# Kernel tuning notes

Measured on AMD Instinct MI355X. Metric: run time of the kernel, lower is better.

## Reference

```python
import jax, jax.numpy as jnp
import numpy as np


def setup_inputs() -> dict:
    key = jax.random.key(0)
    kq, kk, kv = jax.random.split(key, 3)
    B, H, S, D = 4, 16, 2048, 64
    q = jax.random.normal(kq, (B, H, S, D), dtype=jnp.float32)
    k = jax.random.normal(kk, (B, H, S, D), dtype=jnp.float32)
    v = jax.random.normal(kv, (B, H, S, D), dtype=jnp.float32)
    return {"q": q, "k": k, "v": v}


def reference(q, k, v):
    # SplitScaleAttend (inference, no mask, no dropout):
    # softmax(q k^T / sqrt(d)) v — the chunked loop in the original is a
    # memory-saving schedule of the same math, so one fused expression here.
    scale = q.shape[-1] ** (-0.5)
    # (b h i d),(b h j d) -> (b h i j)
    sim = jnp.einsum("bhid,bhjd->bhij", q, k * scale)
    attn = jax.nn.softmax(sim, axis=-1)
    # (b h i j),(b h j d) -> (b h i d)
    return jnp.einsum("bhij,bhjd->bhid", attn, v)
```

## Files before the change

### kernel.cpp

```cpp
#include <hip/hip_runtime.h>
#include <hip/hip_bf16.h>

typedef __attribute__((ext_vector_type(8))) short short8_t;
typedef __attribute__((ext_vector_type(4))) float f32x4;
typedef __attribute__((ext_vector_type(16))) float f32x16;
typedef __attribute__((ext_vector_type(4))) unsigned u32x4;

static constexpr int B = 4, H = 16, S = 2048, D = 64;
static constexpr int WAVES = 8, QW = 64, QBLK = WAVES * QW;
static constexpr int KVBLK = 64, NT = S / KVBLK;
static constexpr int LDK = 72;

#define QSCALE 0.18033688011112042f

__device__ __forceinline__ unsigned pk2(float a, float b) {
    __hip_bfloat162 h = __float22bfloat162_rn(float2{a, b});
    unsigned u;
    __builtin_memcpy(&u, &h, 4);
    return u;
}

__device__ __forceinline__ float fexp2(float x) {
#if __has_builtin(__builtin_amdgcn_exp2f)
    return __builtin_amdgcn_exp2f(x);
#else
    return exp2f(x);
#endif
}

__device__ __forceinline__ float frcp(float x) {
#if __has_builtin(__builtin_amdgcn_rcpf)
    return __builtin_amdgcn_rcpf(x);
#else
    return 1.f / x;
#endif
}

#define QK_MFMA(KH, S0, S1)                                                              \
    do {                                                                                 \
        _Pragma("unroll")                                                                \
        for (int kc = 0; kc < 4; ++kc) {                                                 \
            const short8_t ka = *reinterpret_cast<const short8_t*>(                      \
                &Ks[cb][(KH) * 32 + ql][kc * 16 + hi * 8]);                              \
            S0 = __builtin_amdgcn_mfma_f32_32x32x16_bf16(ka, qf0[kc], S0, 0, 0, 0);      \
            S1 = __builtin_amdgcn_mfma_f32_32x32x16_bf16(ka, qf1[kc], S1, 0, 0, 0);      \
        }                                                                                \
    } while (0)

#define EXP_SUM_PACK(S0, S1, CD0, CD1)                                                   \
    do {                                                                                 \
        float a0 = 0.f, a1 = 0.f, b0 = 0.f, b1 = 0.f;                                    \
        _Pragma("unroll")                                                                \
        for (int r = 0; r < 16; ++r) {                                                   \
            const float e = fexp2(S0[r]);                                                \
            S0[r] = e;                                                                   \
            if (r & 1) a1 += e; else a0 += e;                                            \
        }                                                                                \
        _Pragma("unroll")                                                                \
        for (int r = 0; r < 16; ++r) {                                                   \
            const float e = fexp2(S1[r]);                                                \
            S1[r] = e;                                                                   \
            if (r & 1) b1 += e; else b0 += e;                                            \
        }                                                                                \
        l0_r += a0 + a1;                                                                 \
        l1_r += b0 + b1;                                                                 \
        _Pragma("unroll")                                                                \
        for (int jj = 0; jj < 8; ++jj) {                                                 \
            CD0[jj] = pk2(S0[jj * 2], S0[jj * 2 + 1]);                                   \
            CD1[jj] = pk2(S1[jj * 2], S1[jj * 2 + 1]);                                   \
        }                                                                                \
    } while (0)

#define PV2(CD0, CD1, KS)                                                                \
    do {                                                                                 \
        const int h_ = (KS) & 1;                                                         \
        const short8_t vfa =                                                             \
            *reinterpret_cast<const short8_t*>(&Vt[cb][ql][(KS) * 16 + hi * 8]);         \
        const short8_t vfb =                                                             \
            *reinterpret_cast<const short8_t*>(&Vt[cb][32 + ql][(KS) * 16 + hi * 8]);    \
        {                                                                                \
            unsigned x0 = CD0[4 * h_ + 0], y0 = CD0[4 * h_ + 2];                         \
            unsigned x1 = CD0[4 * h_ + 1], y1 = CD0[4 * h_ + 3];                         \
            asm volatile("v_permlane32_swap_b32 %0, %1" : "+v"(x0), "+v"(y0));           \
            asm volatile("v_permlane32_swap_b32 %0, %1" : "+v"(x1), "+v"(y1));           \
            const u32x4 pu = {x0, x1, y0, y1};                                           \
            const short8_t pa = __builtin_bit_cast(short8_t, pu);                        \
            Od00 = __builtin_amdgcn_mfma_f32_32x32x16_bf16(pa, vfa, Od00, 0, 0, 0);      \
            Od01 = __builtin_amdgcn_mfma_f32_32x32x16_bf16(pa, vfb, Od01, 0, 0, 0);      \
        }                                                                                \
        {                                                                                \
            unsigned x0 = CD1[4 * h_ + 0], y0 = CD1[4 * h_ + 2];                         \
            unsigned x1 = CD1[4 * h_ + 1], y1 = CD1[4 * h_ + 3];                         \
            asm volatile("v_permlane32_swap_b32 %0, %1" : "+v"(x0), "+v"(y0));           \
            asm volatile("v_permlane32_swap_b32 %0, %1" : "+v"(x1), "+v"(y1));           \
            const u32x4 pu = {x0, x1, y0, y1};                                           \
            const short8_t pa = __builtin_bit_cast(short8_t, pu);                        \
            Od10 = __builtin_amdgcn_mfma_f32_32x32x16_bf16(pa, vfa, Od10, 0, 0, 0);      \
            Od11 = __builtin_amdgcn_mfma_f32_32x32x16_bf16(pa, vfb, Od11, 0, 0, 0);      \
        }                                                                                \
    } while (0)

__global__ void __launch_bounds__(512, 2)
attn_fwd(const float* __restrict__ q, const float* __restrict__ k,
         const float* __restrict__ v, float* __restrict__ out) {
    __shared__ short Ks[2][KVBLK][LDK];
    __shared__ short Vt[2][D][LDK];
    __shared__ float Xl[WAVES][2][32];

    const int tid  = threadIdx.x;
    const int lane = tid & 63;
    const int ql   = lane & 31;
    const int hi   = lane >> 5;
    const int wave = tid >> 6;

    const int lid = blockIdx.x;
    const int bh  = (lid & 7) | ((lid >> 5) << 3);
    const int qx  = (lid >> 3) & 3;

    const long base = (long)bh * S * D;
    const int  q0w  = qx * QBLK + wave * QW;

    short8_t qf0[4], qf1[4];
    #pragma unroll
    for (int qb = 0; qb < 2; ++qb) {
        const float* qp = q + base + (long)(q0w + qb * 32 + ql) * D;
        #pragma unroll
        for (int kc = 0; kc < 4; ++kc) {
            const f32x4 a = *reinterpret_cast<const f32x4*>(qp + kc * 16 + hi * 8);
            const f32x4 b = *reinterpret_cast<const f32x4*>(qp + kc * 16 + hi * 8 + 4);
            const u32x4 u = {pk2(a[0] * QSCALE, a[1] * QSCALE),
                             pk2(a[2] * QSCALE, a[3] * QSCALE),
                             pk2(b[0] * QSCALE, b[1] * QSCALE),
                             pk2(b[2] * QSCALE, b[3] * QSCALE)};
            if (qb == 0) qf0[kc] = __builtin_bit_cast(short8_t, u);
            else         qf1[kc] = __builtin_bit_cast(short8_t, u);
        }
    }

    f32x16 Od00, Od01, Od10, Od11;
    #pragma unroll
    for (int r = 0; r < 16; ++r) {
        Od00[r] = 0.f; Od01[r] = 0.f;
        Od10[r] = 0.f; Od11[r] = 0.f;
    }
    float l0_r = 0.f, l1_r = 0.f;

    const int kr  = tid >> 3,       kc0 = (tid & 7) * 8;
    const int vk2 = (tid & 31) * 2, vd0 = (tid >> 5) * 4;
    const float* kptr  = k + base + (long)kr * D + kc0;
    const float* vptrA = v + base + (long)vk2 * D + vd0;

    f32x4 kfa = *reinterpret_cast<const f32x4*>(kptr);
    f32x4 kfb = *reinterpret_cast<const f32x4*>(kptr + 4);
    f32x4 vfa0 = *reinterpret_cast<const f32x4*>(vptrA);
    f32x4 vfb0 = *reinterpret_cast<const f32x4*>(vptrA + D);

    for (int t = 0; t < NT; ++t) {
        const int cb = t & 1;
        {
            const u32x4 ku = {pk2(kfa[0], kfa[1]), pk2(kfa[2], kfa[3]),
                              pk2(kfb[0], kfb[1]), pk2(kfb[2], kfb[3])};
            *reinterpret_cast<u32x4*>(&Ks[cb][kr][kc0]) = ku;
            #pragma unroll
            for (int j = 0; j < 4; ++j) {
                *reinterpret_cast<unsigned*>(&Vt[cb][vd0 + j][vk2]) = pk2(vfa0[j], vfb0[j]);
            }
        }
        __syncthreads();

        if (t + 1 < NT) {
            kptr  += KVBLK * D;
            vptrA += KVBLK * D;
            kfa = *reinterpret_cast<const f32x4*>(kptr);
            kfb = *reinterpret_cast<const f32x4*>(kptr + 4);
            vfa0 = *reinterpret_cast<const f32x4*>(vptrA);
            vfb0 = *reinterpret_cast<const f32x4*>(vptrA + D);
        }

        f32x16 sA0, sA1, sB0, sB1;
        #pragma unroll
        for (int r = 0; r < 16; ++r) { sA0[r] = 0.f; sA1[r] = 0.f; sB0[r] = 0.f; sB1[r] = 0.f; }
        QK_MFMA(0, sA0, sA1);
        QK_MFMA(1, sB0, sB1);

        unsigned cdA0[8], cdA1[8];
        EXP_SUM_PACK(sA0, sA1, cdA0, cdA1);
        PV2(cdA0, cdA1, 0);
        PV2(cdA0, cdA1, 1);

        unsigned cdB0[8], cdB1[8];
        EXP_SUM_PACK(sB0, sB1, cdB0, cdB1);
        PV2(cdB0, cdB1, 2);
        PV2(cdB0, cdB1, 3);
    }

    {
        const float l0m = l0_r + __shfl_xor(l0_r, 32, 64);
        const float l1m = l1_r + __shfl_xor(l1_r, 32, 64);
        if (hi == 0) {
            Xl[wave][0][ql] = frcp(l0m);
            Xl[wave][1][ql] = frcp(l1m);
        }
        float* op = out + base + (long)q0w * D + ql;
        #pragma unroll
        for (int r = 0; r < 16; ++r) {
            const int   row = (r & 3) + 8 * (r >> 2) + 4 * hi;
            const float s   = Xl[wave][0][row];
            op[(long)row * D]      = Od00[r] * s;
            op[(long)row * D + 32] = Od01[r] * s;
        }
        float* op1 = op + 32 * D;
        #pragma unroll
        for (int r = 0; r < 16; ++r) {
            const int   row = (r & 3) + 8 * (r >> 2) + 4 * hi;
            const float s   = Xl[wave][1][row];
            op1[(long)row * D]      = Od10[r] * s;
            op1[(long)row * D + 32] = Od11[r] * s;
        }
    }
}

extern "C" void kernel_launch(void* const* d_in, const int* in_sizes, int n_in,
                              void* d_out, int out_size, void* d_ws, size_t ws_size,
                              hipStream_t stream) {
    const float* q = (const float*)d_in[0];
    const float* k = (const float*)d_in[1];
    const float* v = (const float*)d_in[2];
    float* out = (float*)d_out;
    attn_fwd<<<dim3((S / QBLK) * B * H), 512, 0, stream>>>(q, k, v, out);
}
```

Baseline: 86.24 us.

## Split KV range across two blocks and combine partial outputs in a second kernel

Splits each query block's key/value sequence into two halves processed by separate blocks, doubling the grid to fill more CU slots. Each half writes unnormalized partial outputs in bf16 and row sums to a workspace, and a combine kernel adds them and normalizes. The aim is to lift occupancy and utilization on the large GPU. The cost is extra workspace traffic, an extra launch and bf16 rounding of the partials. The new path is used only when a large enough workspace is provided.

Measured after the change: 100.4 us. 1.16x slower.

```diff
diff --git a/kernel.cpp b/kernel.cpp
--- a/kernel.cpp
+++ b/kernel.cpp
@@ -2,6 +2,7 @@
 #include <hip/hip_bf16.h>
 
 typedef __attribute__((ext_vector_type(8))) short short8_t;
+typedef __attribute__((ext_vector_type(4))) short short4_t;
 typedef __attribute__((ext_vector_type(4))) float f32x4;
 typedef __attribute__((ext_vector_type(16))) float f32x16;
 typedef __attribute__((ext_vector_type(4))) unsigned u32x4;
@@ -9,7 +10,13 @@
 static constexpr int B = 4, H = 16, S = 2048, D = 64;
 static constexpr int WAVES = 8, QW = 64, QBLK = WAVES * QW;
 static constexpr int KVBLK = 64, NT = S / KVBLK;
+static constexpr int NTH = NT / 2;
 static constexpr int LDK = 72;
+
+static constexpr long   ROWS        = (long)B * H * S;
+static constexpr size_t OPART_BYTES = 2ul * ROWS * 64 * 2;
+static constexpr size_t L_OFF       = OPART_BYTES;
+static constexpr size_t WS_NEED     = L_OFF + 2ul * ROWS * 4;
 
 #define QSCALE 0.18033688011112042f
 
@@ -18,6 +25,18 @@
     unsigned u;
     __builtin_memcpy(&u, &h, 4);
     return u;
+}
+__device__ __forceinline__ short bf1(float a) {
+    __hip_bfloat16 h = __float2bfloat16(a);
+    short s;
+    __builtin_memcpy(&s, &h, 2);
+    return s;
+}
+__device__ __forceinline__ float bf2f(short s) {
+    const unsigned u = ((unsigned)(unsigned short)s) << 16;
+    float f;
+    __builtin_memcpy(&f, &u, 4);
+    return f;
 }
 
 __device__ __forceinline__ float fexp2(float x) {
@@ -100,6 +119,139 @@
         }                                                                                \
     } while (0)
 
+#define ATTN_BODY(NTILES, KVOFF)                                                         \
+    short8_t qf0[4], qf1[4];                                                             \
+    _Pragma("unroll")                                                                    \
+    for (int qb = 0; qb < 2; ++qb) {                                                     \
+        const float* qp = q + base + (long)(q0w + qb * 32 + ql) * D;                     \
+        _Pragma("unroll")                                                                \
+        for (int kc = 0; kc < 4; ++kc) {                                                 \
+            const f32x4 a = *reinterpret_cast<const f32x4*>(qp + kc * 16 + hi * 8);      \
+            const f32x4 b = *reinterpret_cast<const f32x4*>(qp + kc * 16 + hi * 8 + 4);  \
+            const u32x4 u = {pk2(a[0] * QSCALE, a[1] * QSCALE),                          \
+                             pk2(a[2] * QSCALE, a[3] * QSCALE),                          \
+                             pk2(b[0] * QSCALE, b[1] * QSCALE),                          \
+                             pk2(b[2] * QSCALE, b[3] * QSCALE)};                         \
+            if (qb == 0) qf0[kc] = __builtin_bit_cast(short8_t, u);                      \
+            else         qf1[kc] = __builtin_bit_cast(short8_t, u);                      \
+        }                                                                                \
+    }                                                                                    \
+    _Pragma("unroll")                                                                    \
+    for (int r = 0; r < 16; ++r) {                                                       \
+        Od00[r] = 0.f; Od01[r] = 0.f;                                                    \
+        Od10[r] = 0.f; Od11[r] = 0.f;                                                    \
+    }                                                                                    \
+    const int kr  = tid >> 3,       kc0 = (tid & 7) * 8;                                 \
+    const int vk2 = (tid & 31) * 2, vd0 = (tid >> 5) * 4;                                \
+    const float* kptr  = k + base + (KVOFF) + (long)kr * D + kc0;                        \
+    const float* vptrA = v + base + (KVOFF) + (long)vk2 * D + vd0;                       \
+    f32x4 kfa = *reinterpret_cast<const f32x4*>(kptr);                                   \
+    f32x4 kfb = *reinterpret_cast<const f32x4*>(kptr + 4);                               \
+    f32x4 vfa0 = *reinterpret_cast<const f32x4*>(vptrA);                                 \
+    f32x4 vfb0 = *reinterpret_cast<const f32x4*>(vptrA + D);                             \
+    for (int t = 0; t < (NTILES); ++t) {                                                 \
+        const int cb = t & 1;                                                            \
+        {                                                                                \
+            const u32x4 ku = {pk2(kfa[0], kfa[1]), pk2(kfa[2], kfa[3]),                  \
+                              pk2(kfb[0], kfb[1]), pk2(kfb[2], kfb[3])};                 \
+            *reinterpret_cast<u32x4*>(&Ks[cb][kr][kc0]) = ku;                            \
+            _Pragma("unroll")                                                            \
+            for (int j = 0; j < 4; ++j) {                                                \
+                *reinterpret_cast<unsigned*>(&Vt[cb][vd0 + j][vk2]) =                    \
+                    pk2(vfa0[j], vfb0[j]);                                               \
+            }                                                                            \
+        }                                                                                \
+        __syncthreads();                                                                 \
+        if (t + 1 < (NTILES)) {                                                          \
+            kptr  += KVBLK * D;                                                          \
+            vptrA += KVBLK * D;                                                          \
+            kfa = *reinterpret_cast<const f32x4*>(kptr);                                 \
+            kfb = *reinterpret_cast<const f32x4*>(kptr + 4);                             \
+            vfa0 = *reinterpret_cast<const f32x4*>(vptrA);                               \
+            vfb0 = *reinterpret_cast<const f32x4*>(vptrA + D);                           \
+        }                                                                                \
+        f32x16 sA0, sA1, sB0, sB1;                                                       \
+        _Pragma("unroll")                                                                \
+        for (int r = 0; r < 16; ++r) {                                                   \
+            sA0[r] = 0.f; sA1[r] = 0.f; sB0[r] = 0.f; sB1[r] = 0.f;                      \
+        }                                                                                \
+        QK_MFMA(0, sA0, sA1);                                                            \
+        QK_MFMA(1, sB0, sB1);                                                            \
+        unsigned cdA0[8], cdA1[8];                                                       \
+        EXP_SUM_PACK(sA0, sA1, cdA0, cdA1);                                              \
+        PV2(cdA0, cdA1, 0);                                                              \
+        PV2(cdA0, cdA1, 1);                                                              \
+        unsigned cdB0[8], cdB1[8];                                                       \
+        EXP_SUM_PACK(sB0, sB1, cdB0, cdB1);                                              \
+        PV2(cdB0, cdB1, 2);                                                              \
+        PV2(cdB0, cdB1, 3);                                                              \
+    }
+
+__global__ void __launch_bounds__(512, 2)
+attn_partial(const float* __restrict__ q, const float* __restrict__ k,
+             const float* __restrict__ v, void* __restrict__ ws) {
+    __shared__ short Ks[2][KVBLK][LDK];
+    __shared__ short Vt[2][D][LDK];
+
+    const int tid  = threadIdx.x;
+    const int lane = tid & 63;
+    const int ql   = lane & 31;
+    const int hi   = lane >> 5;
+    const int wave = tid >> 6;
+
+    const int lid   = blockIdx.x;
+    const int bh    = (lid & 7) | ((lid >> 6) << 3);
+    const int mid   = (lid >> 3) & 7;
+    const int qx    = mid & 3;
+    const int halfk = mid >> 2;
+
+    const long base = (long)bh * S * D;
+    const int  q0w  = qx * QBLK + wave * QW;
+
+    f32x16 Od00, Od01, Od10, Od11;
+    float l0_r = 0.f, l1_r = 0.f;
+
+    ATTN_BODY(NTH, (long)halfk * NTH * KVBLK * D)
+
+    {
+        const float l0m = l0_r + __shfl_xor(l0_r, 32, 64);
+        const float l1m = l1_r + __shfl_xor(l1_r, 32, 64);
+        const long rowbase = (long)bh * S + q0w;
+        float* l_ws = (float*)((char*)ws + L_OFF) + (long)halfk * ROWS;
+        if (hi == 0) {
+            l_ws[rowbase + ql]      = l0m;
+            l_ws[rowbase + 32 + ql] = l1m;
+        }
+        short* o_ws = (short*)ws + ((long)halfk * ROWS + rowbase) * 64;
+        #pragma unroll
+        for (int r = 0; r < 16; ++r) {
+            const int row = (r & 3) + 8 * (r >> 2) + 4 * hi;
+            o_ws[(long)row * 64 + ql]             = bf1(Od00[r]);
+            o_ws[(long)row * 64 + 32 + ql]        = bf1(Od01[r]);
+            o_ws[(long)(row + 32) * 64 + ql]      = bf1(Od10[r]);
+            o_ws[(long)(row + 32) * 64 + 32 + ql] = bf1(Od11[r]);
+        }
+    }
+}
+
+__global__ void __launch_bounds__(256)
+combine_k(const void* __restrict__ ws, float* __restrict__ out) {
+    const long idx = (long)blockIdx.x * 256 + threadIdx.x;
+    const long j4  = idx * 4;
+    const long row = idx >> 4;
+    const short* Oa = (const short*)ws;
+    const short* Ob = Oa + ROWS * 64;
+    const float* la = (const float*)((const char*)ws + L_OFF);
+    const float* lb = la + ROWS;
+    const short4_t a = *reinterpret_cast<const short4_t*>(Oa + j4);
+    const short4_t b = *reinterpret_cast<const short4_t*>(Ob + j4);
+    const float inv = frcp(la[row] + lb[row]);
+    f32x4 o;
+    #pragma unroll
+    for (int j = 0; j < 4; ++j) o[j] = (bf2f(a[j]) + bf2f(b[j])) * inv;
+    *reinterpret_cast<f32x4*>(out + j4) = o;
+}
+
 __global__ void __launch_bounds__(512, 2)
 attn_fwd(const float* __restrict__ q, const float* __restrict__ k,
          const float* __restrict__ v, float* __restrict__ out) {
@@ -120,79 +272,10 @@
     const long base = (long)bh * S * D;
     const int  q0w  = qx * QBLK + wave * QW;
 
-    short8_t qf0[4], qf1[4];
-    #pragma unroll
-    for (int qb = 0; qb < 2; ++qb) {
-        const float* qp = q + base + (long)(q0w + qb * 32 + ql) * D;
-        #pragma unroll
-        for (int kc = 0; kc < 4; ++kc) {
-            const f32x4 a = *reinterpret_cast<const f32x4*>(qp + kc * 16 + hi * 8);
-            const f32x4 b = *reinterpret_cast<const f32x4*>(qp + kc * 16 + hi * 8 + 4);
-            const u32x4 u = {pk2(a[0] * QSCALE, a[1] * QSCALE),
-                             pk2(a[2] * QSCALE, a[3] * QSCALE),
-                             pk2(b[0] * QSCALE, b[1] * QSCALE),
-                             pk2(b[2] * QSCALE, b[3] * QSCALE)};
-            if (qb == 0) qf0[kc] = __builtin_bit_cast(short8_t, u);
-            else         qf1[kc] = __builtin_bit_cast(short8_t, u);
-        }
-    }
-
     f32x16 Od00, Od01, Od10, Od11;
-    #pragma unroll
-    for (int r = 0; r < 16; ++r) {
-        Od00[r] = 0.f; Od01[r] = 0.f;
-        Od10[r] = 0.f; Od11[r] = 0.f;
-    }
     float l0_r = 0.f, l1_r = 0.f;
 
-    const int kr  = tid >> 3,       kc0 = (tid & 7) * 8;
-    const int vk2 = (tid & 31) * 2, vd0 = (tid >> 5) * 4;
-    const float* kptr  = k + base + (long)kr * D + kc0;
-    const float* vptrA = v + base + (long)vk2 * D + vd0;
-
-    f32x4 kfa = *reinterpret_cast<const f32x4*>(kptr);
-    f32x4 kfb = *reinterpret_cast<const f32x4*>(kptr + 4);
-    f32x4 vfa0 = *reinterpret_cast<const f32x4*>(vptrA);
-    f32x4 vfb0 = *reinterpret_cast<const f32x4*>(vptrA + D);
-
-    for (int t = 0; t < NT; ++t) {
-        const int cb = t & 1;
-        {
-            const u32x4 ku = {pk2(kfa[0], kfa[1]), pk2(kfa[2], kfa[3]),
-                              pk2(kfb[0], kfb[1]), pk2(kfb[2], kfb[3])};
-            *reinterpret_cast<u32x4*>(&Ks[cb][kr][kc0]) = ku;
-            #pragma unroll
-            for (int j = 0; j < 4; ++j) {
-                *reinterpret_cast<unsigned*>(&Vt[cb][vd0 + j][vk2]) = pk2(vfa0[j], vfb0[j]);
-            }
-        }
-        __syncthreads();
-
-        if (t + 1 < NT) {
-            kptr  += KVBLK * D;
-            vptrA += KVBLK * D;
-            kfa = *reinterpret_cast<const f32x4*>(kptr);
-            kfb = *reinterpret_cast<const f32x4*>(kptr + 4);
-            vfa0 = *reinterpret_cast<const f32x4*>(vptrA);
-            vfb0 = *reinterpret_cast<const f32x4*>(vptrA + D);
-        }
-
-        f32x16 sA0, sA1, sB0, sB1;
-        #pragma unroll
-        for (int r = 0; r < 16; ++r) { sA0[r] = 0.f; sA1[r] = 0.f; sB0[r] = 0.f; sB1[r] = 0.f; }
-        QK_MFMA(0, sA0, sA1);
-        QK_MFMA(1, sB0, sB1);
-
-        unsigned cdA0[8], cdA1[8];
-        EXP_SUM_PACK(sA0, sA1, cdA0, cdA1);
-        PV2(cdA0, cdA1, 0);
-        PV2(cdA0, cdA1, 1);
-
-        unsigned cdB0[8], cdB1[8];
-        EXP_SUM_PACK(sB0, sB1, cdB0, cdB1);
-        PV2(cdB0, cdB1, 2);
-        PV2(cdB0, cdB1, 3);
-    }
+    ATTN_BODY(NT, 0)
 
     {
         const float l0m = l0_r + __shfl_xor(l0_r, 32, 64);
@@ -227,5 +310,10 @@
     const float* k = (const float*)d_in[1];
     const float* v = (const float*)d_in[2];
     float* out = (float*)d_out;
-    attn_fwd<<<dim3((S / QBLK) * B * H), 512, 0, stream>>>(q, k, v, out);
-}
+    if (ws_size >= WS_NEED && d_ws != nullptr) {
+        attn_partial<<<dim3(2 * (S / QBLK) * B * H), 512, 0, stream>>>(q, k, v, d_ws);
+        combine_k<<<dim3((unsigned)(ROWS * 64 / 4 / 256)), 256, 0, stream>>>(d_ws, out);
+    } else {
+        attn_fwd<<<dim3((S / QBLK) * B * H), 512, 0, stream>>>(q, k, v, out);
+    }
+}
```
